# Optimization experiments

Hardware: AMD Instinct MI355X
Metric: run time of the kernel (lower is better)

## Reference

```python
import jax, jax.numpy as jnp
import numpy as np

N = 100_000   # nodes
E = 3_200_000 # edges (avg degree 32)
H = 128       # hidden units
G = 64        # graphs in batch
EPS = 1e-5    # BatchNorm eps


def setup_inputs() -> dict:
    key = jax.random.key(0)
    ks = jax.random.split(key, 32)
    s = 0.05
    inp = {
        "x": jax.random.normal(ks[0], (N, 1), dtype=jnp.float32),
        "edge_index": jax.random.randint(ks[1], (2, E), 0, N, dtype=jnp.int64 if jax.config.jax_enable_x64 else jnp.int32),
        "batch": jnp.sort(jax.random.randint(ks[2], (N,), 0, G, dtype=jnp.int64 if jax.config.jax_enable_x64 else jnp.int32)),
    }
    dims = [(1, H), (H, H), (H, H)]
    k = 3
    for li, (cin, cout) in enumerate(dims, start=1):
        inp[f"W_rel{li}"] = jax.random.normal(ks[k], (cout, cin), dtype=jnp.float32) * s; k += 1
        inp[f"b_rel{li}"] = jax.random.normal(ks[k], (cout,), dtype=jnp.float32) * s; k += 1
        inp[f"W_root{li}"] = jax.random.normal(ks[k], (cout, cin), dtype=jnp.float32) * s; k += 1
        inp[f"gamma{li}"] = jnp.ones((cout,), dtype=jnp.float32)
        inp[f"beta{li}"] = jnp.zeros((cout,), dtype=jnp.float32)
        inp[f"mean{li}"] = jax.random.normal(ks[k], (cout,), dtype=jnp.float32) * s; k += 1
        inp[f"var{li}"] = jax.random.uniform(ks[k], (cout,), dtype=jnp.float32, minval=0.5, maxval=1.5); k += 1
    inp["W_out"] = jax.random.normal(ks[k], (1, H), dtype=jnp.float32) * s; k += 1
    inp["b_out"] = jax.random.normal(ks[k], (1,), dtype=jnp.float32) * s
    return inp


def _graph_conv(x, src, dst, W_rel, b_rel, W_root):
    # PyG GraphConv (aggr='add'): out_i = W_rel @ sum_{j->i} x_j + b_rel + W_root @ x_i
    agg = jax.ops.segment_sum(x[src], dst, num_segments=N)  # [N, Cin]
    return agg @ W_rel.T + b_rel + x @ W_root.T


def _bn_eval(x, gamma, beta, mean, var):
    return (x - mean) * jax.lax.rsqrt(var + EPS) * gamma + beta


def reference(x, edge_index, batch,
              W_rel1, b_rel1, W_root1, gamma1, beta1, mean1, var1,
              W_rel2, b_rel2, W_root2, gamma2, beta2, mean2, var2,
              W_rel3, b_rel3, W_root3, gamma3, beta3, mean3, var3,
              W_out, b_out):
    src, dst = edge_index[0], edge_index[1]
    h = _graph_conv(x, src, dst, W_rel1, b_rel1, W_root1)
    h = jax.nn.relu(_bn_eval(h, gamma1, beta1, mean1, var1))  # dropout p=0 / eval -> identity
    h = _graph_conv(h, src, dst, W_rel2, b_rel2, W_root2)
    h = jax.nn.relu(_bn_eval(h, gamma2, beta2, mean2, var2))
    h = _graph_conv(h, src, dst, W_rel3, b_rel3, W_root3)
    h = _bn_eval(h, gamma3, beta3, mean3, var3)
    # global mean pool over graphs
    sums = jax.ops.segment_sum(h, batch, num_segments=G)                       # [G, H]
    cnts = jax.ops.segment_sum(jnp.ones((N, 1), h.dtype), batch, num_segments=G)
    pooled = sums / jnp.maximum(cnts, 1.0)
    return pooled @ W_out.T + b_out  # [G, 1]
```

## Files before the change

kernel.cpp:

```cpp
#include <hip/hip_runtime.h>

typedef unsigned int uint;
typedef unsigned short ushort;
typedef unsigned char uchar;

#define EPS 1e-5f
#define BSH 8
#define NBMAX 512
#define BCAP 10240
#define SCAT_E 4096

typedef __attribute__((ext_vector_type(8))) short short8;
typedef __attribute__((ext_vector_type(16))) float f32x16;
typedef __attribute__((ext_vector_type(2))) float float2v;
typedef __attribute__((ext_vector_type(2))) _Float16 half2v;
typedef __attribute__((ext_vector_type(8))) _Float16 f16x8;

static __device__ __forceinline__ ushort f2h(float f) {
    return __builtin_bit_cast(ushort, (_Float16)f);
}
static __device__ __forceinline__ half2v u2h(uint u) {
    return __builtin_bit_cast(half2v, u);
}

__global__ __launch_bounds__(256) void bucket_count_kernel(const int* __restrict__ dst,
                                                           int* __restrict__ bcnt, int E, int NB) {
    __shared__ int lh[NBMAX];
    const int tid = threadIdx.x;
    for (int t = tid; t < NB; t += 256) lh[t] = 0;
    __syncthreads();
    const int base = blockIdx.x * 8192, end = min(base + 8192, E);
    for (int i = base + tid; i < end; i += 256) atomicAdd(&lh[dst[i] >> BSH], 1);
    __syncthreads();
    for (int t = tid; t < NB; t += 256) {
        int c = lh[t];
        if (c) atomicAdd(&bcnt[t], c);
    }
}

__global__ void scan_gcur_kernel(const int* __restrict__ bcnt, int* __restrict__ gcur, int nb) {
    int t = threadIdx.x;
    int orig = (t < nb) ? bcnt[t] : 0;
    int v = orig;
    int lane = t & 63, w = t >> 6;
#pragma unroll
    for (int d = 1; d < 64; d <<= 1) { int u = __shfl_up(v, d); if (lane >= d) v += u; }
    __shared__ int wsum[8];
    if (lane == 63) wsum[w] = v;
    __syncthreads();
    int off = 0;
    for (int i = 0; i < w; ++i) off += wsum[i];
    if (t < nb) gcur[t] = off + v - orig;
}

__global__ __launch_bounds__(256) void bucket_scatter_kernel(const int* __restrict__ src,
                                                             const int* __restrict__ dst,
                                                             int* __restrict__ gcur,
                                                             uint* __restrict__ stage,
                                                             int E, int NB) {
    __shared__ int lh[NBMAX];
    __shared__ int lbase[NBMAX];
    const int tid = threadIdx.x;
    const int base = blockIdx.x * SCAT_E;
    const int end = min(base + SCAT_E, E);
    for (int t = tid; t < NB; t += 256) lh[t] = 0;
    __syncthreads();
    for (int i = base + tid; i < end; i += 256) atomicAdd(&lh[dst[i] >> BSH], 1);
    __syncthreads();
    for (int t = tid; t < NB; t += 256) {
        int c = lh[t];
        lbase[t] = c ? atomicAdd(&gcur[t], c) : 0;
        lh[t] = 0;
    }
    __syncthreads();
    for (int i = base + tid; i < end; i += 256) {
        int d = dst[i];
        int b = d >> BSH;
        int pos = lbase[b] + atomicAdd(&lh[b], 1);
        stage[pos] = (uint)src[i] | ((uint)(d & 255) << 17);
    }
}

__global__ __launch_bounds__(256) void bucket_final_kernel(const uint* __restrict__ stage,
                                                           const int* __restrict__ gcur,
                                                           int* __restrict__ rowptr,
                                                           int* __restrict__ eidx, int n) {
    __shared__ uint sbuf[BCAP];
    __shared__ int cnt[256];
    __shared__ int wsum[4];
    const int b = blockIdx.x, tid = threadIdx.x;
    const int r0 = b ? gcur[b - 1] : 0;
    const int r1 = gcur[b];
    const int len = r1 - r0;
    const bool inl = (len <= BCAP);
    cnt[tid] = 0;
    if (inl) for (int i = tid; i < len; i += 256) sbuf[i] = stage[r0 + i];
    __syncthreads();
    for (int i = tid; i < len; i += 256) {
        uint v = inl ? sbuf[i] : stage[r0 + i];
        atomicAdd(&cnt[v >> 17], 1);
    }
    __syncthreads();
    int orig = cnt[tid], v = orig;
    int lane = tid & 63, w = tid >> 6;
#pragma unroll
    for (int d2 = 1; d2 < 64; d2 <<= 1) { int u = __shfl_up(v, d2); if (lane >= d2) v += u; }
    if (lane == 63) wsum[w] = v;
    __syncthreads();
    int off = 0;
    for (int k = 0; k < w; ++k) off += wsum[k];
    const int excl = r0 + off + v - orig;
    const int d = (b << BSH) + tid;
    if (d <= n) rowptr[d] = excl;
    __syncthreads();
    cnt[tid] = excl;
    __syncthreads();
    for (int i = tid; i < len; i += 256) {
        uint pv = inl ? sbuf[i] : stage[r0 + i];
        int slot = atomicAdd(&cnt[pv >> 17], 1);
        eidx[slot] = (int)(pv & 0x1FFFFu);
    }
}

__global__ __launch_bounds__(256) void layer1_fused_kernel(
    const float* __restrict__ x, const int* __restrict__ rowptr, const int* __restrict__ eidx,
    const float* __restrict__ Wrel, const float* __restrict__ brel,
    const float* __restrict__ Wroot, const float* __restrict__ gamma,
    const float* __restrict__ beta, const float* __restrict__ mean,
    const float* __restrict__ var, ushort* __restrict__ h1, int n) {
    __shared__ float A[128], B[128], C[128];
    const int tid = threadIdx.x;
    if (tid < 128) {
        float sc = gamma[tid] * rsqrtf(var[tid] + EPS);
        A[tid] = Wrel[tid] * sc;
        B[tid] = Wroot[tid] * sc;
        C[tid] = beta[tid] + (brel[tid] - mean[tid]) * sc;
    }
    __syncthreads();
    const int g16 = tid >> 4;
    const int l16 = tid & 15;
    const int node = blockIdx.x * 16 + g16;
    if (node >= n) return;
    const int e0 = rowptr[node], e1 = rowptr[node + 1];
    float acc = 0.f;
    for (int e = e0 + l16; e < e1; e += 16) acc += x[eidx[e]];
#pragma unroll
    for (int d = 1; d < 16; d <<= 1) acc += __shfl_xor(acc, d);
    const float xi = x[node];
    uint4 o;
    ushort* op = (ushort*)&o;
#pragma unroll
    for (int j = 0; j < 8; ++j) {
        int c = l16 * 8 + j;
        op[j] = f2h(fmaxf(acc * A[c] + xi * B[c] + C[c], 0.f));
    }
    *((uint4*)(h1 + (size_t)node * 128) + l16) = o;
}

__global__ __launch_bounds__(256) void f16_to_fp8_kernel(const ushort* __restrict__ h,
                                                         uint* __restrict__ h8, int total4) {
    int i = blockIdx.x * 256 + threadIdx.x;
    if (i >= total4) return;
    uint2 u = ((const uint2*)h)[i];
    half2v h0 = u2h(u.x), h1 = u2h(u.y);
    int p = __builtin_amdgcn_cvt_pk_fp8_f32((float)h0[0], (float)h0[1], 0, 0);
    p = __builtin_amdgcn_cvt_pk_fp8_f32((float)h1[0], (float)h1[1], p, 1);
    h8[i] = (uint)p;
}

__global__ __launch_bounds__(256) void gather_fp8_kernel(const uchar* __restrict__ h8,
                                                         const int* __restrict__ rowptr,
                                                         const int* __restrict__ eidx,
                                                         ushort* __restrict__ agg, int n) {
    const int node = blockIdx.x * 4 + (threadIdx.x >> 6);
    if (node >= n) return;
    const int lane = threadIdx.x & 63;
    const int g = lane >> 4;
    const int c8 = lane & 15;
    const uint2* hq = (const uint2*)h8;
    const int e0 = rowptr[node];
    const int len = rowptr[node + 1] - e0;

    float2v a0 = {0.f, 0.f}, a1 = {0.f, 0.f}, a2 = {0.f, 0.f}, a3 = {0.f, 0.f};

#define ACC8(u)                                                        \
    do {                                                               \
        a0 += __builtin_amdgcn_cvt_pk_f32_fp8((int)(u).x, 0);          \
        a1 += __builtin_amdgcn_cvt_pk_f32_fp8((int)(u).x, 1);          \
        a2 += __builtin_amdgcn_cvt_pk_f32_fp8((int)(u).y, 0);          \
        a3 += __builtin_amdgcn_cvt_pk_f32_fp8((int)(u).y, 1);          \
    } while (0)

    for (int base = 0; base < len; base += 64) {
        const int cnt = min(len - base, 64);
        int msrc = (lane < cnt) ? eidx[e0 + base + lane] : 0;
        const int kfull = cnt >> 2;
        int k = 0;
        for (; k + 8 <= kfull; k += 8) {
            uint2 u[8];
#pragma unroll
            for (int s = 0; s < 8; ++s) {
                int src = __shfl(msrc, (k + s) * 4 + g);
                u[s] = hq[(size_t)src * 16 + c8];
            }
#pragma unroll
            for (int s = 0; s < 8; ++s) ACC8(u[s]);
        }
        for (; k < kfull; ++k) {
            int src = __shfl(msrc, k * 4 + g);
            uint2 u = hq[(size_t)src * 16 + c8];
            ACC8(u);
        }
        const int rem = cnt & 3;
        if (rem) {
            int idx = (kfull << 2) + g;
            int src = __shfl(msrc, idx);
            if (g < rem) {
                uint2 u = hq[(size_t)src * 16 + c8];
                ACC8(u);
            }
        }
    }
#undef ACC8

#pragma unroll
    for (int d = 16; d <= 32; d <<= 1) {
        a0[0] += __shfl_xor(a0[0], d); a0[1] += __shfl_xor(a0[1], d);
        a1[0] += __shfl_xor(a1[0], d); a1[1] += __shfl_xor(a1[1], d);
        a2[0] += __shfl_xor(a2[0], d); a2[1] += __shfl_xor(a2[1], d);
        a3[0] += __shfl_xor(a3[0], d); a3[1] += __shfl_xor(a3[1], d);
    }
    if (g == 0) {
        uint4 o;
        ushort* op = (ushort*)&o;
        op[0] = f2h(a0[0]); op[1] = f2h(a0[1]);
        op[2] = f2h(a1[0]); op[3] = f2h(a1[1]);
        op[4] = f2h(a2[0]); op[5] = f2h(a2[1]);
        op[6] = f2h(a3[0]); op[7] = f2h(a3[1]);
        ((uint4*)agg)[(size_t)node * 16 + c8] = o;
    }
}

__global__ void wf_prep_kernel(const float* __restrict__ W0, const float* __restrict__ W1,
                               const float* __restrict__ W2, const float* __restrict__ W3,
                               ushort* __restrict__ WF2, ushort* __restrict__ WF3) {
    int i = blockIdx.x * 256 + threadIdx.x;
    const float* Ws[4] = {W0, W1, W2, W3};
    int mat = i >> 14;
    int m = i & 16383;
    int j = m & 7, lane = (m >> 3) & 63, ct = (m >> 9) & 3, kt = (m >> 11) & 7;
    int row = ct * 32 + (lane & 31);
    int col = kt * 16 + ((lane >> 5) * 8) + j;
    float v = Ws[mat][row * 128 + col];
    ushort* dstp = (mat < 2) ? WF2 : WF3;
    dstp[(mat & 1) * 16384 + m] = f2h(v);
}

template <int RELU>
__global__ __launch_bounds__(256) void conv_mfma_kernel(
    const short* __restrict__ agg, const short* __restrict__ hin,
    const short* __restrict__ WF,
    const float* __restrict__ brel, const float* __restrict__ gamma,
    const float* __restrict__ beta, const float* __restrict__ mean,
    const float* __restrict__ var,
    ushort* __restrict__ hout, int n) {
    const int lane = threadIdx.x & 63;
    const int wt = blockIdx.x * 4 + (threadIdx.x >> 6);
    const int node0 = wt * 32;
    if (node0 >= n) return;
    const int rowA = node0 + (lane & 31);
    const int arow = (rowA < n) ? rowA : (n - 1);
    const int koff = (lane >> 5) * 8;

    f32x16 acc[4];
#pragma unroll
    for (int c = 0; c < 4; ++c) acc[c] = (f32x16)(0.0f);

#pragma unroll
    for (int half = 0; half < 2; ++half) {
        const short* A = (half ? hin : agg) + (size_t)arow * 128 + koff;
        const short* B0 = WF + half * 16384 + lane * 8;
#pragma unroll
        for (int kt = 0; kt < 8; ++kt) {
            f16x8 a = __builtin_bit_cast(f16x8, *(const short8*)(A + kt * 16));
            const short* Bp = B0 + kt * 2048;
#pragma unroll
            for (int ct = 0; ct < 4; ++ct) {
                f16x8 b = __builtin_bit_cast(f16x8, *(const short8*)(Bp + ct * 512));
                acc[ct] = __builtin_amdgcn_mfma_f32_32x32x16_f16(a, b, acc[ct], 0, 0, 0);
            }
        }
    }

#pragma unroll
    for (int ct = 0; ct < 4; ++ct) {
        int c = ct * 32 + (lane & 31);
        float s = gamma[c] * rsqrtf(var[c] + EPS);
        float t = beta[c] - mean[c] * s + brel[c] * s;
#pragma unroll
        for (int r = 0; r < 16; ++r) {
            int row = (r & 3) + 8 * (r >> 2) + 4 * (lane >> 5);
            int node = node0 + row;
            if (node < n) {
                float v = acc[ct][r] * s + t;
                if (RELU) v = fmaxf(v, 0.f);
                hout[(size_t)node * 128 + c] = f2h(v);
            }
        }
    }
}

__global__ __launch_bounds__(256) void pool_kernel(const ushort* __restrict__ h,
                                                   const int* __restrict__ batch,
                                                   const float* __restrict__ Wout,
                                                   float* __restrict__ gscal,
                                                   int* __restrict__ gcnt, int n) {
    const int wv = blockIdx.x * 4 + (threadIdx.x >> 6);
    const int lane = threadIdx.x & 63;
    const int base = wv * 64;
    if (base >= n) return;
    const int end = min(base + 64, n);
    const uint* hu = (const uint*)h;
    const float w0 = Wout[lane * 2], w1 = Wout[lane * 2 + 1];
    float s = 0.f;
    int cur = batch[base], cl = 0;

    auto accum = [&](uint u) {
        half2v hv = u2h(u);
        s += (float)hv[0] * w0 + (float)hv[1] * w1;
        cl++;
    };
    auto flush = [&](int g) {
        float r = s;
#pragma unroll
        for (int d = 1; d < 64; d <<= 1) r += __shfl_xor(r, d);
        if (lane == 0) { atomicAdd(&gscal[g], r); atomicAdd(&gcnt[g], cl); }
        s = 0.f; cl = 0;
    };

    int i = base;
    for (; i + 4 <= end; i += 4) {
        int b3 = batch[i + 3];
        uint u0 = hu[(size_t)i * 64 + lane];
        uint u1 = hu[(size_t)(i + 1) * 64 + lane];
        uint u2 = hu[(size_t)(i + 2) * 64 + lane];
        uint u3 = hu[(size_t)(i + 3) * 64 + lane];
        if (b3 == cur) {
            accum(u0); accum(u1); accum(u2); accum(u3);
        } else {
            int bb[4] = {batch[i], batch[i + 1], batch[i + 2], b3};
            uint uu[4] = {u0, u1, u2, u3};
            for (int k = 0; k < 4; ++k) {
                if (bb[k] != cur) { flush(cur); cur = bb[k]; }
                accum(uu[k]);
            }
        }
    }
    for (; i < end; ++i) {
        int g = batch[i];
        if (g != cur) { flush(cur); cur = g; }
        accum(hu[(size_t)i * 64 + lane]);
    }
    flush(cur);
}

__global__ void out_kernel(const float* __restrict__ gscal, const int* __restrict__ gcnt,
                           const float* __restrict__ bout, float* __restrict__ out, int G) {
    int g = threadIdx.x;
    if (g < G) out[g] = gscal[g] / fmaxf((float)gcnt[g], 1.0f) + bout[0];
}

extern "C" void kernel_launch(void* const* d_in, const int* in_sizes, int n_in,
                              void* d_out, int out_size, void* d_ws, size_t ws_size,
                              hipStream_t stream) {
    const int N = in_sizes[0];
    const int E = in_sizes[1] / 2;
    const int G = 64;

    const float* x     = (const float*)d_in[0];
    const int*   ei    = (const int*)d_in[1];
    const int*   batch = (const int*)d_in[2];
    const int*   src   = ei;
    const int*   dst   = ei + E;

    const float* Wrel1 = (const float*)d_in[3];
    const float* brel1 = (const float*)d_in[4];
    const float* Wroot1= (const float*)d_in[5];
    const float* g1    = (const float*)d_in[6];
    const float* be1   = (const float*)d_in[7];
    const float* m1    = (const float*)d_in[8];
    const float* v1    = (const float*)d_in[9];
    const float* Wrel2 = (const float*)d_in[10];
    const float* brel2 = (const float*)d_in[11];
    const float* Wroot2= (const float*)d_in[12];
    const float* g2    = (const float*)d_in[13];
    const float* be2   = (const float*)d_in[14];
    const float* m2    = (const float*)d_in[15];
    const float* v2    = (const float*)d_in[16];
    const float* Wrel3 = (const float*)d_in[17];
    const float* brel3 = (const float*)d_in[18];
    const float* Wroot3= (const float*)d_in[19];
    const float* g3    = (const float*)d_in[20];
    const float* be3   = (const float*)d_in[21];
    const float* m3    = (const float*)d_in[22];
    const float* v3    = (const float*)d_in[23];
    const float* Wout  = (const float*)d_in[24];
    const float* bout  = (const float*)d_in[25];

    float* out = (float*)d_out;

    char* w = (char*)d_ws;
    auto alloc = [&](size_t bytes) { char* p = w; w += (bytes + 511) & ~(size_t)511; return p; };
    int*    rowptr = (int*)alloc((size_t)(N + 1) * 4);
    int*    bcnt   = (int*)alloc(NBMAX * 4);
    int*    gcur   = (int*)alloc(NBMAX * 4);
    uint*   stage  = (uint*)alloc((size_t)E * 4);
    int*    eidx   = (int*)alloc((size_t)E * 4);
    ushort* hA     = (ushort*)alloc((size_t)N * 128 * 2);
    ushort* hB     = (ushort*)alloc((size_t)N * 128 * 2);
    ushort* aggb   = (ushort*)alloc((size_t)N * 128 * 2);
    uchar*  h8     = (uchar*)alloc((size_t)N * 128);
    ushort* WF2    = (ushort*)alloc(32768 * 2);
    ushort* WF3    = (ushort*)alloc(32768 * 2);
    float*  gscal  = (float*)alloc((size_t)G * 4);
    int*    gcnt   = (int*)alloc((size_t)G * 4);

    const int NB   = (N >> BSH) + 1;
    const int cntBlk  = (E + 8191) / 8192;
    const int scatBlk = (E + SCAT_E - 1) / SCAT_E;

    hipMemsetAsync(bcnt, 0, NBMAX * 4, stream);
    hipMemsetAsync(gscal, 0, (size_t)G * 4, stream);
    hipMemsetAsync(gcnt, 0, (size_t)G * 4, stream);

    bucket_count_kernel<<<cntBlk, 256, 0, stream>>>(dst, bcnt, E, NB);
    scan_gcur_kernel<<<1, 512, 0, stream>>>(bcnt, gcur, NB);
    bucket_scatter_kernel<<<scatBlk, 256, 0, stream>>>(src, dst, gcur, stage, E, NB);
    bucket_final_kernel<<<NB, 256, 0, stream>>>(stage, gcur, rowptr, eidx, N);

    wf_prep_kernel<<<256, 256, 0, stream>>>(Wrel2, Wroot2, Wrel3, Wroot3, WF2, WF3);

    layer1_fused_kernel<<<(N + 15) / 16, 256, 0, stream>>>(x, rowptr, eidx, Wrel1, brel1,
                                                           Wroot1, g1, be1, m1, v1, hA, N);

    const int nwt     = (N + 31) / 32;
    const int convBlk = (nwt + 3) / 4;
    const int gBlk    = (N + 3) / 4;
    const int total4  = N * 32;
    const int cvtBlk  = (total4 + 255) / 256;

    f16_to_fp8_kernel<<<cvtBlk, 256, 0, stream>>>(hA, (uint*)h8, total4);
    gather_fp8_kernel<<<gBlk, 256, 0, stream>>>(h8, rowptr, eidx, aggb, N);
    conv_mfma_kernel<1><<<convBlk, 256, 0, stream>>>((const short*)aggb, (const short*)hA,
                                                     (const short*)WF2, brel2, g2, be2, m2, v2,
                                                     hB, N);

    f16_to_fp8_kernel<<<cvtBlk, 256, 0, stream>>>(hB, (uint*)h8, total4);
    gather_fp8_kernel<<<gBlk, 256, 0, stream>>>(h8, rowptr, eidx, aggb, N);
    conv_mfma_kernel<0><<<convBlk, 256, 0, stream>>>((const short*)aggb, (const short*)hB,
                                                     (const short*)WF3, brel3, g3, be3, m3, v3,
                                                     hA, N);

    pool_kernel<<<(N + 255) / 256, 256, 0, stream>>>(hA, batch, Wout, gscal, gcnt, N);
    out_kernel<<<1, 64, 0, stream>>>(gscal, gcnt, bout, out, G);
}
```

Baseline: 333.7 us.

## Fuse FP8 conversion into producers and stage bucket scatter through shared memory

The standalone f16-to-fp8 kernels are removed. Layer 1 and the first MFMA conv kernel now also write the fp8 copy of their output, computed directly from the f32 values. The bucket scatter kernel first sorts each chunk into shared memory by bucket, then writes contiguous runs to the staging buffer, aiming for more coalesced global stores. Bucket granularity moves to 128 nodes with larger scatter chunks, and the scans are adjusted to match. The cost is per-byte fp8 stores inside the conv epilogue and a binary search per edge during the scatter write-out.

After: 348.5 us. 4.4% more time.

```diff
diff --git a/kernel.cpp b/kernel.cpp
--- a/kernel.cpp
+++ b/kernel.cpp
@@ -5,10 +5,10 @@
 typedef unsigned char uchar;
 
 #define EPS 1e-5f
-#define BSH 8
-#define NBMAX 512
-#define BCAP 10240
-#define SCAT_E 4096
+#define BSH 7
+#define NBMAX 1024
+#define BCAP 6144
+#define SCAT_E 8192
 
 typedef __attribute__((ext_vector_type(8))) short short8;
 typedef __attribute__((ext_vector_type(16))) float f32x16;
@@ -39,18 +39,30 @@
 }
 
 __global__ void scan_gcur_kernel(const int* __restrict__ bcnt, int* __restrict__ gcur, int nb) {
-    int t = threadIdx.x;
-    int orig = (t < nb) ? bcnt[t] : 0;
-    int v = orig;
+    __shared__ int wsum[4];
+    const int t = threadIdx.x;
+    int e[4], s = 0;
+#pragma unroll
+    for (int k = 0; k < 4; ++k) {
+        int idx = t * 4 + k;
+        e[k] = (idx < nb) ? bcnt[idx] : 0;
+        s += e[k];
+    }
     int lane = t & 63, w = t >> 6;
+    int v = s;
 #pragma unroll
     for (int d = 1; d < 64; d <<= 1) { int u = __shfl_up(v, d); if (lane >= d) v += u; }
-    __shared__ int wsum[8];
     if (lane == 63) wsum[w] = v;
     __syncthreads();
     int off = 0;
-    for (int i = 0; i < w; ++i) off += wsum[i];
-    if (t < nb) gcur[t] = off + v - orig;
+    for (int k = 0; k < w; ++k) off += wsum[k];
+    int run = off + v - s;
+#pragma unroll
+    for (int k = 0; k < 4; ++k) {
+        int idx = t * 4 + k;
+        if (idx < nb) gcur[idx] = run;
+        run += e[k];
+    }
 }
 
 __global__ __launch_bounds__(256) void bucket_scatter_kernel(const int* __restrict__ src,
@@ -58,26 +70,59 @@
                                                              int* __restrict__ gcur,
                                                              uint* __restrict__ stage,
                                                              int E, int NB) {
+    __shared__ uint sedge[SCAT_E];
     __shared__ int lh[NBMAX];
+    __shared__ int lofs[NBMAX + 1];
     __shared__ int lbase[NBMAX];
+    __shared__ int wsum[4];
     const int tid = threadIdx.x;
     const int base = blockIdx.x * SCAT_E;
-    const int end = min(base + SCAT_E, E);
+    const int len = min(base + SCAT_E, E) - base;
+
     for (int t = tid; t < NB; t += 256) lh[t] = 0;
     __syncthreads();
-    for (int i = base + tid; i < end; i += 256) atomicAdd(&lh[dst[i] >> BSH], 1);
-    __syncthreads();
-    for (int t = tid; t < NB; t += 256) {
-        int c = lh[t];
-        lbase[t] = c ? atomicAdd(&gcur[t], c) : 0;
-        lh[t] = 0;
-    }
-    __syncthreads();
-    for (int i = base + tid; i < end; i += 256) {
-        int d = dst[i];
+    for (int i = tid; i < len; i += 256) atomicAdd(&lh[dst[base + i] >> BSH], 1);
+    __syncthreads();
+    int e[4], s = 0;
+#pragma unroll
+    for (int k = 0; k < 4; ++k) {
+        int idx = tid * 4 + k;
+        e[k] = (idx < NB) ? lh[idx] : 0;
+        s += e[k];
+    }
+    int lane = tid & 63, w = tid >> 6;
+    int v = s;
+#pragma unroll
+    for (int d = 1; d < 64; d <<= 1) { int u = __shfl_up(v, d); if (lane >= d) v += u; }
+    if (lane == 63) wsum[w] = v;
+    __syncthreads();
+    int off = 0;
+    for (int k = 0; k < w; ++k) off += wsum[k];
+    int run = off + v - s;
+#pragma unroll
+    for (int k = 0; k < 4; ++k) {
+        int idx = tid * 4 + k;
+        if (idx <= NB) lofs[idx] = run;
+        if (idx < NB && e[k]) lbase[idx] = atomicAdd(&gcur[idx], e[k]);
+        run += e[k];
+    }
+    __syncthreads();
+    for (int t = tid; t < NB; t += 256) lh[t] = 0;
+    __syncthreads();
+    for (int i = tid; i < len; i += 256) {
+        int d = dst[base + i];
         int b = d >> BSH;
-        int pos = lbase[b] + atomicAdd(&lh[b], 1);
-        stage[pos] = (uint)src[i] | ((uint)(d & 255) << 17);
+        int r = atomicAdd(&lh[b], 1);
+        sedge[lofs[b] + r] = (uint)src[base + i] | ((uint)(d & 127) << 17);
+    }
+    __syncthreads();
+    for (int i = tid; i < len; i += 256) {
+        int lo = 0, hi = NB;
+        while (hi - lo > 1) {
+            int mid = (lo + hi) >> 1;
+            if (lofs[mid] <= i) lo = mid; else hi = mid;
+        }
+        stage[lbase[lo] + (i - lofs[lo])] = sedge[i];
     }
 }
 
@@ -86,14 +131,14 @@
                                                            int* __restrict__ rowptr,
                                                            int* __restrict__ eidx, int n) {
     __shared__ uint sbuf[BCAP];
-    __shared__ int cnt[256];
-    __shared__ int wsum[4];
+    __shared__ int cnt[128];
+    __shared__ int wsum[2];
     const int b = blockIdx.x, tid = threadIdx.x;
     const int r0 = b ? gcur[b - 1] : 0;
     const int r1 = gcur[b];
     const int len = r1 - r0;
     const bool inl = (len <= BCAP);
-    cnt[tid] = 0;
+    if (tid < 128) cnt[tid] = 0;
     if (inl) for (int i = tid; i < len; i += 256) sbuf[i] = stage[r0 + i];
     __syncthreads();
     for (int i = tid; i < len; i += 256) {
@@ -101,19 +146,23 @@
         atomicAdd(&cnt[v >> 17], 1);
     }
     __syncthreads();
-    int orig = cnt[tid], v = orig;
-    int lane = tid & 63, w = tid >> 6;
-#pragma unroll
-    for (int d2 = 1; d2 < 64; d2 <<= 1) { int u = __shfl_up(v, d2); if (lane >= d2) v += u; }
-    if (lane == 63) wsum[w] = v;
-    __syncthreads();
-    int off = 0;
-    for (int k = 0; k < w; ++k) off += wsum[k];
-    const int excl = r0 + off + v - orig;
-    const int d = (b << BSH) + tid;
-    if (d <= n) rowptr[d] = excl;
-    __syncthreads();
-    cnt[tid] = excl;
+    int excl = 0, orig = 0, v = 0;
+    if (tid < 128) {
+        orig = cnt[tid]; v = orig;
+        int lane = tid & 63;
+#pragma unroll
+        for (int d2 = 1; d2 < 64; d2 <<= 1) { int u = __shfl_up(v, d2); if (lane >= d2) v += u; }
+        if (lane == 63) wsum[tid >> 6] = v;
+    }
+    __syncthreads();
+    if (tid < 128) {
+        int off = (tid >= 64) ? wsum[0] : 0;
+        excl = r0 + off + v - orig;
+        int d = (b << BSH) + tid;
+        if (d <= n) rowptr[d] = excl;
+    }
+    __syncthreads();
+    if (tid < 128) cnt[tid] = excl;
     __syncthreads();
     for (int i = tid; i < len; i += 256) {
         uint pv = inl ? sbuf[i] : stage[r0 + i];
@@ -127,7 +176,7 @@
     const float* __restrict__ Wrel, const float* __restrict__ brel,
     const float* __restrict__ Wroot, const float* __restrict__ gamma,
     const float* __restrict__ beta, const float* __restrict__ mean,
-    const float* __restrict__ var, ushort* __restrict__ h1, int n) {
+    const float* __restrict__ var, ushort* __restrict__ h1, uchar* __restrict__ h8, int n) {
     __shared__ float A[128], B[128], C[128];
     const int tid = threadIdx.x;
     if (tid < 128) {
@@ -147,25 +196,23 @@
 #pragma unroll
     for (int d = 1; d < 16; d <<= 1) acc += __shfl_xor(acc, d);
     const float xi = x[node];
+    float vv[8];
     uint4 o;
     ushort* op = (ushort*)&o;
 #pragma unroll
     for (int j = 0; j < 8; ++j) {
         int c = l16 * 8 + j;
-        op[j] = f2h(fmaxf(acc * A[c] + xi * B[c] + C[c], 0.f));
+        vv[j] = fmaxf(acc * A[c] + xi * B[c] + C[c], 0.f);
+        op[j] = f2h(vv[j]);
     }
     *((uint4*)(h1 + (size_t)node * 128) + l16) = o;
-}
-
-__global__ __launch_bounds__(256) void f16_to_fp8_kernel(const ushort* __restrict__ h,
-                                                         uint* __restrict__ h8, int total4) {
-    int i = blockIdx.x * 256 + threadIdx.x;
-    if (i >= total4) return;
-    uint2 u = ((const uint2*)h)[i];
-    half2v h0 = u2h(u.x), h1 = u2h(u.y);
-    int p = __builtin_amdgcn_cvt_pk_fp8_f32((float)h0[0], (float)h0[1], 0, 0);
-    p = __builtin_amdgcn_cvt_pk_fp8_f32((float)h1[0], (float)h1[1], p, 1);
-    h8[i] = (uint)p;
+    uint p0 = 0, p1 = 0;
+    p0 = __builtin_amdgcn_cvt_pk_fp8_f32(vv[0], vv[1], 0, 0);
+    p0 = __builtin_amdgcn_cvt_pk_fp8_f32(vv[2], vv[3], p0, 1);
+    p1 = __builtin_amdgcn_cvt_pk_fp8_f32(vv[4], vv[5], 0, 0);
+    p1 = __builtin_amdgcn_cvt_pk_fp8_f32(vv[6], vv[7], p1, 1);
+    uint2 o8; o8.x = p0; o8.y = p1;
+    ((uint2*)(h8 + (size_t)node * 128))[l16] = o8;
 }
 
 __global__ __launch_bounds__(256) void gather_fp8_kernel(const uchar* __restrict__ h8,
@@ -256,14 +303,14 @@
     dstp[(mat & 1) * 16384 + m] = f2h(v);
 }
 
-template <int RELU>
+template <int RELU, int WRITE8>
 __global__ __launch_bounds__(256) void conv_mfma_kernel(
     const short* __restrict__ agg, const short* __restrict__ hin,
     const short* __restrict__ WF,
     const float* __restrict__ brel, const float* __restrict__ gamma,
     const float* __restrict__ beta, const float* __restrict__ mean,
     const float* __restrict__ var,
-    ushort* __restrict__ hout, int n) {
+    ushort* __restrict__ hout, uchar* __restrict__ h8out, int n) {
     const int lane = threadIdx.x & 63;
     const int wt = blockIdx.x * 4 + (threadIdx.x >> 6);
     const int node0 = wt * 32;
@@ -305,6 +352,10 @@
                 float v = acc[ct][r] * s + t;
                 if (RELU) v = fmaxf(v, 0.f);
                 hout[(size_t)node * 128 + c] = f2h(v);
+                if (WRITE8) {
+                    uint p = __builtin_amdgcn_cvt_pk_fp8_f32(v, v, 0, 0);
+                    h8out[(size_t)node * 128 + c] = (uchar)p;
+                }
             }
         }
     }
@@ -425,7 +476,7 @@
     float*  gscal  = (float*)alloc((size_t)G * 4);
     int*    gcnt   = (int*)alloc((size_t)G * 4);
 
-    const int NB   = (N >> BSH) + 1;
+    const int NB      = (N >> BSH) + 1;
     const int cntBlk  = (E + 8191) / 8192;
     const int scatBlk = (E + SCAT_E - 1) / SCAT_E;
 
@@ -434,32 +485,28 @@
     hipMemsetAsync(gcnt, 0, (size_t)G * 4, stream);
 
     bucket_count_kernel<<<cntBlk, 256, 0, stream>>>(dst, bcnt, E, NB);
-    scan_gcur_kernel<<<1, 512, 0, stream>>>(bcnt, gcur, NB);
+    scan_gcur_kernel<<<1, 256, 0, stream>>>(bcnt, gcur, NB);
     bucket_scatter_kernel<<<scatBlk, 256, 0, stream>>>(src, dst, gcur, stage, E, NB);
     bucket_final_kernel<<<NB, 256, 0, stream>>>(stage, gcur, rowptr, eidx, N);
 
     wf_prep_kernel<<<256, 256, 0, stream>>>(Wrel2, Wroot2, Wrel3, Wroot3, WF2, WF3);
 
     layer1_fused_kernel<<<(N + 15) / 16, 256, 0, stream>>>(x, rowptr, eidx, Wrel1, brel1,
-                                                           Wroot1, g1, be1, m1, v1, hA, N);
+                                                           Wroot1, g1, be1, m1, v1, hA, h8, N);
 
     const int nwt     = (N + 31) / 32;
     const int convBlk = (nwt + 3) / 4;
     const int gBlk    = (N + 3) / 4;
-    const int total4  = N * 32;
-    const int cvtBlk  = (total4 + 255) / 256;
-
-    f16_to_fp8_kernel<<<cvtBlk, 256, 0, stream>>>(hA, (uint*)h8, total4);
+
     gather_fp8_kernel<<<gBlk, 256, 0, stream>>>(h8, rowptr, eidx, aggb, N);
-    conv_mfma_kernel<1><<<convBlk, 256, 0, stream>>>((const short*)aggb, (const short*)hA,
-                                                     (const short*)WF2, brel2, g2, be2, m2, v2,
-                                                     hB, N);
-
-    f16_to_fp8_kernel<<<cvtBlk, 256, 0, stream>>>(hB, (uint*)h8, total4);
+    conv_mfma_kernel<1, 1><<<convBlk, 256, 0, stream>>>((const short*)aggb, (const short*)hA,
+                                                        (const short*)WF2, brel2, g2, be2, m2, v2,
+                                                        hB, h8, N);
+
     gather_fp8_kernel<<<gBlk, 256, 0, stream>>>(h8, rowptr, eidx, aggb, N);
-    conv_mfma_kernel<0><<<convBlk, 256, 0, stream>>>((const short*)aggb, (const short*)hB,
-                                                     (const short*)WF3, brel3, g3, be3, m3, v3,
-                                                     hA, N);
+    conv_mfma_kernel<0, 0><<<convBlk, 256, 0, stream>>>((const short*)aggb, (const short*)hB,
+                                                        (const short*)WF3, brel3, g3, be3, m3, v3,
+                                                        hA, (uchar*)nullptr, N);
 
     pool_kernel<<<(N + 255) / 256, 256, 0, stream>>>(hA, batch, Wout, gscal, gcnt, N);
     out_kernel<<<1, 64, 0, stream>>>(gscal, gcnt, bout, out, G);
```
